# Optimization experiments

Measured on AMD Instinct MI355X. Metric: run time of the kernel, lower is better.

The kernel has to match this reference:

```python
import jax, jax.numpy as jnp
import numpy as np
from jax import lax


def _gru(x, h, Wih, Whh, bih, bhh):
    # PyTorch GRU cell: gates order (r, z, n)
    gi = x @ Wih.T + bih
    gh = h @ Whh.T + bhh
    ir, iz, inn = jnp.split(gi, 3, axis=-1)
    hr, hz, hn = jnp.split(gh, 3, axis=-1)
    r = jax.nn.sigmoid(ir + hr)
    z = jax.nn.sigmoid(iz + hz)
    n = jnp.tanh(inn + r * hn)
    return (1.0 - z) * n + z * h


def setup_inputs() -> dict:
    key = jax.random.key(0)
    ks = jax.random.split(key, 20)
    B, T, D, H, V, S = 128, 80, 4096, 1024, 6000, 10
    s = 0.02
    inp = {
        "data": jax.random.normal(ks[0], (B, T, D), dtype=jnp.float32),
        "mask": jnp.ones((B, S), dtype=jnp.float32),
        "target": jax.random.randint(ks[1], (B, S), 0, V),
        "sent_len": S,
        "enc_Wih": jax.random.normal(ks[2], (3 * H, D), dtype=jnp.float32) * s,
        "enc_Whh": jax.random.normal(ks[3], (3 * H, H), dtype=jnp.float32) * s,
        "enc_bih": jax.random.normal(ks[4], (3 * H,), dtype=jnp.float32) * s,
        "enc_bhh": jax.random.normal(ks[5], (3 * H,), dtype=jnp.float32) * s,
        "dec_Wih": jax.random.normal(ks[6], (3 * H, H), dtype=jnp.float32) * s,
        "dec_Whh": jax.random.normal(ks[7], (3 * H, H), dtype=jnp.float32) * s,
        "dec_bih": jax.random.normal(ks[8], (3 * H,), dtype=jnp.float32) * s,
        "dec_bhh": jax.random.normal(ks[9], (3 * H,), dtype=jnp.float32) * s,
        "lin1_W": jax.random.normal(ks[10], (H, 2 * H), dtype=jnp.float32) * s,
        "lin1_b": jnp.zeros((H,), dtype=jnp.float32),
        "lin2_W": jax.random.normal(ks[11], (V, H), dtype=jnp.float32) * s,
        "lin2_b": jnp.zeros((V,), dtype=jnp.float32),
        "embed": jax.random.normal(ks[12], (V, H), dtype=jnp.float32) * s,
    }
    return inp


def reference(data, mask, target, sent_len,
              enc_Wih, enc_Whh, enc_bih, enc_bhh,
              dec_Wih, dec_Whh, dec_bih, dec_bhh,
              lin1_W, lin1_b, lin2_W, lin2_b, embed):
    B = data.shape[0]
    H = lin1_b.shape[0]
    W1a = lin1_W[:, :H]   # acts on encoder hidden half
    W1b = lin1_W[:, H:]   # acts on embedded word half

    eh0 = jnp.zeros((B, H), dtype=data.dtype)
    dh0 = jnp.zeros((B, H), dtype=data.dtype)

    # ---- encode phase: feed video features; decoder sees [enc_hid, 0] ----
    def enc_step(carry, x_t):
        eh, dh = carry
        eh = _gru(x_t, eh, enc_Wih, enc_Whh, enc_bih, enc_bhh)
        u = jax.nn.relu(eh @ W1a.T + lin1_b)  # zeros half contributes nothing
        dh = _gru(u, dh, dec_Wih, dec_Whh, dec_bih, dec_bhh)
        return (eh, dh), None

    (eh, dh), _ = lax.scan(enc_step, (eh0, dh0), jnp.swapaxes(data, 0, 1))

    # ---- decode phase: encoder input is zeros; decoder sees [enc_hid, embed(word)] ----
    ir0, iz0, in0 = jnp.split(enc_bih, 3)  # zero-input encoder gates

    def dec_step(carry, tgt_t):
        eh, dh, word = carry
        gh = eh @ enc_Whh.T + enc_bhh
        hr, hz, hn = jnp.split(gh, 3, axis=-1)
        r = jax.nn.sigmoid(ir0 + hr)
        z = jax.nn.sigmoid(iz0 + hz)
        n = jnp.tanh(in0 + r * hn)
        eh = (1.0 - z) * n + z * eh

        emb = embed[word]  # [B, H]
        u = jax.nn.relu(eh @ W1a.T + emb @ W1b.T + lin1_b)
        dh = _gru(u, dh, dec_Wih, dec_Whh, dec_bih, dec_bhh)
        logp = jax.nn.log_softmax(dh @ lin2_W.T + lin2_b, axis=-1)  # [B, V]
        new_word = jnp.argmax(logp, axis=1).astype(jnp.int32)
        loss_t = -jnp.mean(logp[jnp.arange(B), tgt_t])  # NLLLoss (mask unused, as in source)
        return (eh, dh, new_word), (loss_t, new_word[0], new_word[1])

    word0 = jnp.ones((B,), dtype=jnp.int32)
    (_, _, _), (losses, sent, sent2) = lax.scan(dec_step, (eh, dh, word0), jnp.swapaxes(target, 0, 1))
    return jnp.sum(losses), sent, sent2
```

## Files before the change

kernel.cpp:

```cpp
#include <hip/hip_runtime.h>
#include <math.h>
#include <float.h>

#define B_ 128
#define T_ 80
#define D_ 4096
#define H_ 1024
#define V_ 6000
#define S_ 10
#define G3 (3*H_)
#define KSPLIT 4

typedef unsigned short ushort_t;
typedef __attribute__((ext_vector_type(8))) unsigned short u16x8;
typedef __attribute__((ext_vector_type(8))) short s16x8;
typedef __attribute__((ext_vector_type(4))) float fx4;

__device__ float    g_gi[(size_t)B_*T_*G3];
__device__ ushort_t g_Ah[(size_t)B_*T_*D_];
__device__ ushort_t g_Al[(size_t)B_*T_*D_];
__device__ ushort_t g_Bh[(size_t)G3*D_];
__device__ ushort_t g_Bl[(size_t)G3*D_];
__device__ float g_ghp [KSPLIT*B_*G3];
__device__ float g_gi2p[KSPLIT*B_*G3];
__device__ float g_gh2p[KSPLIT*B_*G3];
__device__ float g_up  [KSPLIT*B_*H_];
__device__ float g_eh[B_*H_];
__device__ float g_dh[B_*H_];
__device__ float g_u[B_*H_];
__device__ float g_cat[B_*2*H_];
__device__ float g_logits[B_*V_];
__device__ int   g_word[B_];

__device__ inline void split1(float x, ushort_t& hi, ushort_t& lo) {
    unsigned u = __float_as_uint(x);
    unsigned rh = u + 0x7FFF + ((u >> 16) & 1);
    hi = (ushort_t)(rh >> 16);
    float fhi = __uint_as_float((unsigned)hi << 16);
    float d = x - fhi;
    unsigned u2 = __float_as_uint(d);
    unsigned rl = u2 + 0x7FFF + ((u2 >> 16) & 1);
    lo = (ushort_t)(rl >> 16);
}

__global__ __launch_bounds__(256) void split_bf16(
    const float* __restrict__ x, ushort_t* __restrict__ hi,
    ushort_t* __restrict__ lo, int n4)
{
    int i = blockIdx.x * 256 + threadIdx.x;
    if (i >= n4) return;
    float4 v = ((const float4*)x)[i];
    ushort_t h0,h1,h2,h3,l0,l1,l2,l3;
    split1(v.x,h0,l0); split1(v.y,h1,l1); split1(v.z,h2,l2); split1(v.w,h3,l3);
    u16x8 dummy;
    ushort_t* hp = hi + (size_t)i*4;  hp[0]=h0; hp[1]=h1; hp[2]=h2; hp[3]=h3;
    ushort_t* lp = lo + (size_t)i*4;  lp[0]=l0; lp[1]=l1; lp[2]=l2; lp[3]=l3;
    (void)dummy;
}

__global__ __launch_bounds__(256) void gemm_mfma_x3(
    const ushort_t* __restrict__ Ahg, const ushort_t* __restrict__ Alg,
    const ushort_t* __restrict__ Bhg, const ushort_t* __restrict__ Blg,
    const float* __restrict__ bias, float* __restrict__ C, int N, int K)
{
    __shared__ ushort_t sAh[128*32], sAl[128*32], sBh[128*32], sBl[128*32];
    const int tid  = threadIdx.x;
    const int bm   = blockIdx.y * 128, bn = blockIdx.x * 128;
    const int wave = tid >> 6, lane = tid & 63;
    const int wr   = (wave >> 1) * 64, wc = (wave & 1) * 64;
    const int r    = lane & 15, g = lane >> 4;

    fx4 acc[4][4] = {};

    for (int k0 = 0; k0 < K; k0 += 32) {
        __syncthreads();
#pragma unroll
        for (int i = 0; i < 2; ++i) {
            const int o   = (tid + i*256) * 16;
            const int row = o >> 6;
            const int el  = (o & 63) >> 1;
            const size_t ga = (size_t)(bm + row) * K + k0 + el;
            const size_t gb = (size_t)(bn + row) * K + k0 + el;
            u16x8 vah = *(const u16x8*)(Ahg + ga);
            u16x8 val = *(const u16x8*)(Alg + ga);
            u16x8 vbh = *(const u16x8*)(Bhg + gb);
            u16x8 vbl = *(const u16x8*)(Blg + gb);
            const int lo2 = o >> 1;
            *(u16x8*)&sAh[lo2] = vah;
            *(u16x8*)&sAl[lo2] = val;
            *(u16x8*)&sBh[lo2] = vbh;
            *(u16x8*)&sBl[lo2] = vbl;
        }
        __syncthreads();

        s16x8 ah[4], al[4], bh[4], bl[4];
#pragma unroll
        for (int i = 0; i < 4; ++i) {
            const int ao = (wr + i*16 + r)*32 + g*8;
            const int bo = (wc + i*16 + r)*32 + g*8;
            ah[i] = *(const s16x8*)&sAh[ao];
            al[i] = *(const s16x8*)&sAl[ao];
            bh[i] = *(const s16x8*)&sBh[bo];
            bl[i] = *(const s16x8*)&sBl[bo];
        }
#pragma unroll
        for (int i = 0; i < 4; ++i)
#pragma unroll
            for (int j = 0; j < 4; ++j) {
                acc[i][j] = __builtin_amdgcn_mfma_f32_16x16x32_bf16(ah[i], bh[j], acc[i][j], 0, 0, 0);
                acc[i][j] = __builtin_amdgcn_mfma_f32_16x16x32_bf16(al[i], bh[j], acc[i][j], 0, 0, 0);
                acc[i][j] = __builtin_amdgcn_mfma_f32_16x16x32_bf16(ah[i], bl[j], acc[i][j], 0, 0, 0);
            }
    }

#pragma unroll
    for (int i = 0; i < 4; ++i)
#pragma unroll
        for (int j = 0; j < 4; ++j)
#pragma unroll
            for (int reg = 0; reg < 4; ++reg) {
                const int row = bm + wr + i*16 + g*4 + reg;
                const int col = bn + wc + j*16 + r;
                C[(size_t)row * N + col] = acc[i][j][reg] + bias[col];
            }
}

#define BM 64
#define BN 64
#define BK 16

__global__ __launch_bounds__(256) void gemm_wt(
    const float* __restrict__ A, int lda,
    const float* __restrict__ W, int ldw,
    const float* __restrict__ bias,
    float* __restrict__ C, int ldc,
    int M, int N, int K)
{
    __shared__ float As[BK][BM];
    __shared__ float Ws[BK][BN];
    const int tid = threadIdx.x;
    const int bm = blockIdx.y * BM;
    const int bn = blockIdx.x * BN;
    const int lr = tid >> 2;
    const int lc = (tid & 3) << 2;
    const int tr = (tid >> 4) << 2;
    const int tc = (tid & 15) << 2;

    float acc[4][4] = {};
    for (int k0 = 0; k0 < K; k0 += BK) {
        {
            const int gr = bm + lr;
            float4 av = *(const float4*)(A + (size_t)gr * lda + k0 + lc);
            As[lc+0][lr] = av.x; As[lc+1][lr] = av.y;
            As[lc+2][lr] = av.z; As[lc+3][lr] = av.w;
            const int wr2 = bn + lr;
            float4 wv = make_float4(0.f,0.f,0.f,0.f);
            if (wr2 < N) wv = *(const float4*)(W + (size_t)wr2 * ldw + k0 + lc);
            Ws[lc+0][lr] = wv.x; Ws[lc+1][lr] = wv.y;
            Ws[lc+2][lr] = wv.z; Ws[lc+3][lr] = wv.w;
        }
        __syncthreads();
#pragma unroll
        for (int k = 0; k < BK; ++k) {
            float4 a4 = *(const float4*)&As[k][tr];
            float4 b4 = *(const float4*)&Ws[k][tc];
            float ar[4] = {a4.x,a4.y,a4.z,a4.w};
            float br[4] = {b4.x,b4.y,b4.z,b4.w};
#pragma unroll
            for (int i = 0; i < 4; ++i)
#pragma unroll
                for (int j = 0; j < 4; ++j)
                    acc[i][j] = fmaf(ar[i], br[j], acc[i][j]);
        }
        __syncthreads();
    }
#pragma unroll
    for (int i = 0; i < 4; ++i) {
        const int m = bm + tr + i;
#pragma unroll
        for (int j = 0; j < 4; ++j) {
            const int n = bn + tc + j;
            if (n < N) C[(size_t)m * ldc + n] = acc[i][j] + bias[n];
        }
    }
}

__global__ __launch_bounds__(256) void gemm_wt_sk(
    const float* __restrict__ A, int lda,
    const float* __restrict__ W, int ldw,
    float* __restrict__ Cp,
    const float* __restrict__ A2,
    const float* __restrict__ W2,
    float* __restrict__ Cp2,
    int M, int N, int K)
{
    const int z = blockIdx.z;
    const int s = z & (KSPLIT - 1);
    if (z >= KSPLIT) { A = A2; W = W2; Cp = Cp2; }

    __shared__ float As[BK][BM];
    __shared__ float Ws[BK][BN];
    const int tid = threadIdx.x;
    const int bm = blockIdx.y * BM;
    const int bn = blockIdx.x * BN;
    const int lr = tid >> 2;
    const int lc = (tid & 3) << 2;
    const int tr = (tid >> 4) << 2;
    const int tc = (tid & 15) << 2;
    const int kc = K / KSPLIT;
    const int kbeg = s * kc;

    float acc[4][4] = {};
    for (int k0 = kbeg; k0 < kbeg + kc; k0 += BK) {
        {
            const int gr = bm + lr;
            float4 av = *(const float4*)(A + (size_t)gr * lda + k0 + lc);
            As[lc+0][lr] = av.x; As[lc+1][lr] = av.y;
            As[lc+2][lr] = av.z; As[lc+3][lr] = av.w;
            const int wr2 = bn + lr;
            float4 wv = *(const float4*)(W + (size_t)wr2 * ldw + k0 + lc);
            Ws[lc+0][lr] = wv.x; Ws[lc+1][lr] = wv.y;
            Ws[lc+2][lr] = wv.z; Ws[lc+3][lr] = wv.w;
        }
        __syncthreads();
#pragma unroll
        for (int k = 0; k < BK; ++k) {
            float4 a4 = *(const float4*)&As[k][tr];
            float4 b4 = *(const float4*)&Ws[k][tc];
            float ar[4] = {a4.x,a4.y,a4.z,a4.w};
            float br[4] = {b4.x,b4.y,b4.z,b4.w};
#pragma unroll
            for (int i = 0; i < 4; ++i)
#pragma unroll
                for (int j = 0; j < 4; ++j)
                    acc[i][j] = fmaf(ar[i], br[j], acc[i][j]);
        }
        __syncthreads();
    }
    float* Cs = Cp + (size_t)s * M * N;
#pragma unroll
    for (int i = 0; i < 4; ++i) {
        const int m = bm + tr + i;
#pragma unroll
        for (int j = 0; j < 4; ++j)
            Cs[(size_t)m * N + bn + tc + j] = acc[i][j];
    }
}

__global__ __launch_bounds__(256) void gru_update2(
    const float* __restrict__ GI, int gi_rstride, int gi_nsplit,
    const float* __restrict__ bih,
    const float* __restrict__ GHp, const float* __restrict__ bhh,
    float* __restrict__ h)
{
    const int idx = blockIdx.x * 256 + threadIdx.x;
    const int b = idx >> 10;
    const int j = idx & (H_ - 1);
    float ir, iz, inn;
    if (gi_nsplit == 0) {
        const float* gi = GI + (size_t)b * gi_rstride;
        ir = gi[j]; iz = gi[H_ + j]; inn = gi[2*H_ + j];
    } else {
        ir = bih[j]; iz = bih[H_ + j]; inn = bih[2*H_ + j];
        const float* p = GI + (size_t)b * G3;
#pragma unroll
        for (int s = 0; s < KSPLIT; ++s) {
            ir += p[j]; iz += p[H_ + j]; inn += p[2*H_ + j];
            p += (size_t)B_ * G3;
        }
    }
    float hr = bhh[j], hz = bhh[H_ + j], hn = bhh[2*H_ + j];
    const float* q = GHp + (size_t)b * G3;
#pragma unroll
    for (int s = 0; s < KSPLIT; ++s) {
        hr += q[j]; hz += q[H_ + j]; hn += q[2*H_ + j];
        q += (size_t)B_ * G3;
    }
    const float rg = 1.f / (1.f + expf(-(ir + hr)));
    const float zg = 1.f / (1.f + expf(-(iz + hz)));
    const float ng = tanhf(inn + rg * hn);
    h[idx] = (1.f - zg) * ng + zg * h[idx];
}

__global__ __launch_bounds__(256) void relu_combine(
    const float* __restrict__ Up, const float* __restrict__ bias,
    float* __restrict__ u)
{
    const int idx = blockIdx.x * 256 + threadIdx.x;
    const int j = idx & (H_ - 1);
    float v = bias[j];
#pragma unroll
    for (int s = 0; s < KSPLIT; ++s) v += Up[(size_t)s * B_ * H_ + idx];
    u[idx] = fmaxf(v, 0.f);
}

__global__ __launch_bounds__(256) void cat_eh_emb(
    const float* __restrict__ eh, const float* __restrict__ embed,
    const int* __restrict__ word, float* __restrict__ cat)
{
    const int idx = blockIdx.x * 256 + threadIdx.x;
    const int b = idx >> 11;
    const int j = idx & (2*H_ - 1);
    float v;
    if (j < H_) v = eh[b * H_ + j];
    else        v = embed[(size_t)word[b] * H_ + (j - H_)];
    cat[idx] = v;
}

__global__ __launch_bounds__(256) void init_state(
    float* __restrict__ eh, float* __restrict__ dh,
    int* __restrict__ word, float* __restrict__ out)
{
    const int idx = blockIdx.x * 256 + threadIdx.x;
    if (idx < B_*H_) { eh[idx] = 0.f; dh[idx] = 0.f; }
    if (idx < B_)    word[idx] = 1;
    if (idx < 21)    out[idx] = 0.f;
}

__global__ __launch_bounds__(256) void softmax_loss(
    const float* __restrict__ logits, const int* __restrict__ target,
    int s, int* __restrict__ word, float* __restrict__ out)
{
    const int b = blockIdx.x;
    const int t = threadIdx.x;
    const float* row = logits + (size_t)b * V_;
    __shared__ float sv[256];
    __shared__ int   si[256];
    __shared__ float ss[256];

    float best = -FLT_MAX; int bi = 0;
    for (int j = t; j < V_; j += 256) {
        float v = row[j];
        if (v > best) { best = v; bi = j; }
    }
    sv[t] = best; si[t] = bi;
    __syncthreads();
    for (int off = 128; off > 0; off >>= 1) {
        if (t < off) {
            float v2 = sv[t + off]; int i2 = si[t + off];
            if (v2 > sv[t] || (v2 == sv[t] && i2 < si[t])) { sv[t] = v2; si[t] = i2; }
        }
        __syncthreads();
    }
    const float m = sv[0];
    const int amax = si[0];

    float sum = 0.f;
    for (int j = t; j < V_; j += 256) sum += expf(row[j] - m);
    ss[t] = sum;
    __syncthreads();
    for (int off = 128; off > 0; off >>= 1) {
        if (t < off) ss[t] += ss[t + off];
        __syncthreads();
    }
    if (t == 0) {
        const float lse = m + logf(ss[0]);
        const int tgt = target[b * S_ + s];
        const float logp = row[tgt] - lse;
        atomicAdd(&out[0], -logp * (1.0f / (float)B_));
        word[b] = amax;
        if (b == 0) out[1 + s]  = (float)amax;
        if (b == 1) out[11 + s] = (float)amax;
    }
}

extern "C" void kernel_launch(void* const* d_in, const int* in_sizes, int n_in,
                              void* d_out, int out_size, void* d_ws, size_t ws_size,
                              hipStream_t stream)
{
    const float* data    = (const float*)d_in[0];
    const int*   target  = (const int*)  d_in[2];
    const float* enc_Wih = (const float*)d_in[4];
    const float* enc_Whh = (const float*)d_in[5];
    const float* enc_bih = (const float*)d_in[6];
    const float* enc_bhh = (const float*)d_in[7];
    const float* dec_Wih = (const float*)d_in[8];
    const float* dec_Whh = (const float*)d_in[9];
    const float* dec_bih = (const float*)d_in[10];
    const float* dec_bhh = (const float*)d_in[11];
    const float* lin1_W  = (const float*)d_in[12];
    const float* lin1_b  = (const float*)d_in[13];
    const float* lin2_W  = (const float*)d_in[14];
    const float* lin2_b  = (const float*)d_in[15];
    const float* embed   = (const float*)d_in[16];
    float* out = (float*)d_out;

    float *gi, *eh, *dh, *u, *cat, *logits, *ghp, *gi2p, *gh2p, *up;
    ushort_t *Ah, *Al, *Bh, *Bl; int* word;
    hipGetSymbolAddress((void**)&gi,     HIP_SYMBOL(g_gi));
    hipGetSymbolAddress((void**)&Ah,     HIP_SYMBOL(g_Ah));
    hipGetSymbolAddress((void**)&Al,     HIP_SYMBOL(g_Al));
    hipGetSymbolAddress((void**)&Bh,     HIP_SYMBOL(g_Bh));
    hipGetSymbolAddress((void**)&Bl,     HIP_SYMBOL(g_Bl));
    hipGetSymbolAddress((void**)&ghp,    HIP_SYMBOL(g_ghp));
    hipGetSymbolAddress((void**)&gi2p,   HIP_SYMBOL(g_gi2p));
    hipGetSymbolAddress((void**)&gh2p,   HIP_SYMBOL(g_gh2p));
    hipGetSymbolAddress((void**)&up,     HIP_SYMBOL(g_up));
    hipGetSymbolAddress((void**)&eh,     HIP_SYMBOL(g_eh));
    hipGetSymbolAddress((void**)&dh,     HIP_SYMBOL(g_dh));
    hipGetSymbolAddress((void**)&u,      HIP_SYMBOL(g_u));
    hipGetSymbolAddress((void**)&cat,    HIP_SYMBOL(g_cat));
    hipGetSymbolAddress((void**)&logits, HIP_SYMBOL(g_logits));
    hipGetSymbolAddress((void**)&word,   HIP_SYMBOL(g_word));

    init_state<<<512, 256, 0, stream>>>(eh, dh, word, out);

    split_bf16<<<(B_*T_*D_/4 + 255)/256, 256, 0, stream>>>(data,    Ah, Al, B_*T_*D_/4);
    split_bf16<<<(G3*D_/4   + 255)/256, 256, 0, stream>>>(enc_Wih, Bh, Bl, G3*D_/4);

    {
        dim3 grid(G3/128, (B_*T_)/128, 1);
        gemm_mfma_x3<<<grid, 256, 0, stream>>>(Ah, Al, Bh, Bl, enc_bih, gi, G3, D_);
    }

    for (int t = 0; t < T_; ++t) {
        { dim3 grid(G3/BN, B_/BM, KSPLIT);
          gemm_wt_sk<<<grid, 256, 0, stream>>>(eh, H_, enc_Whh, H_, ghp,
                                               nullptr, nullptr, nullptr, B_, G3, H_); }
        gru_update2<<<512, 256, 0, stream>>>(gi + (size_t)t * G3, T_ * G3, 0, nullptr,
                                             ghp, enc_bhh, eh);
        { dim3 grid(H_/BN, B_/BM, KSPLIT);
          gemm_wt_sk<<<grid, 256, 0, stream>>>(eh, H_, lin1_W, 2*H_, up,
                                               nullptr, nullptr, nullptr, B_, H_, H_); }
        relu_combine<<<512, 256, 0, stream>>>(up, lin1_b, u);
        { dim3 grid(G3/BN, B_/BM, 2*KSPLIT);
          gemm_wt_sk<<<grid, 256, 0, stream>>>(u, H_, dec_Wih, H_, gi2p,
                                               dh, dec_Whh, gh2p, B_, G3, H_); }
        gru_update2<<<512, 256, 0, stream>>>(gi2p, 0, KSPLIT, dec_bih,
                                             gh2p, dec_bhh, dh);
    }

    for (int s = 0; s < S_; ++s) {
        { dim3 grid(G3/BN, B_/BM, KSPLIT);
          gemm_wt_sk<<<grid, 256, 0, stream>>>(eh, H_, enc_Whh, H_, ghp,
                                               nullptr, nullptr, nullptr, B_, G3, H_); }
        gru_update2<<<512, 256, 0, stream>>>(enc_bih, 0, 0, nullptr,
                                             ghp, enc_bhh, eh);
        cat_eh_emb<<<1024, 256, 0, stream>>>(eh, embed, word, cat);
        { dim3 grid(H_/BN, B_/BM, KSPLIT);
          gemm_wt_sk<<<grid, 256, 0, stream>>>(cat, 2*H_, lin1_W, 2*H_, up,
                                               nullptr, nullptr, nullptr, B_, H_, 2*H_); }
        relu_combine<<<512, 256, 0, stream>>>(up, lin1_b, u);
        { dim3 grid(G3/BN, B_/BM, 2*KSPLIT);
          gemm_wt_sk<<<grid, 256, 0, stream>>>(u, H_, dec_Wih, H_, gi2p,
                                               dh, dec_Whh, gh2p, B_, G3, H_); }
        gru_update2<<<512, 256, 0, stream>>>(gi2p, 0, KSPLIT, dec_bih,
                                             gh2p, dec_bhh, dh);
        { dim3 grid((V_+BN-1)/BN, B_/BM, 1);
          gemm_wt<<<grid, 256, 0, stream>>>(dh, H_, lin2_W, H_, lin2_b, logits, V_, B_, V_, H_); }
        softmax_loss<<<B_, 256, 0, stream>>>(logits, target, s, word, out);
    }
}
```

Measured before the change: 8.728 ms.

## Move recurrent GEMMs to split-bf16 MFMA with double-buffered LDS loads

Replaces the fp32 FMA split-K GEMMs for the per-step recurrent matmuls with the 3-pass bf16 hi/lo MFMA kernel, generalized for split-K, leading dimensions and a dual-problem launch. Weights are pre-split once and hidden states are split inside the elementwise update kernels. The MFMA kernel now double-buffers shared memory using direct global-to-LDS loads, which should overlap loads with compute for the big input GEMM too. With M=128 the recurrent GEMMs launch few 128x128 tiles, so occupancy may be low, and the extra split work adds memory traffic.

```diff
diff --git a/kernel.cpp b/kernel.cpp
--- a/kernel.cpp
+++ b/kernel.cpp
@@ -12,7 +12,6 @@
 #define KSPLIT 4
 
 typedef unsigned short ushort_t;
-typedef __attribute__((ext_vector_type(8))) unsigned short u16x8;
 typedef __attribute__((ext_vector_type(8))) short s16x8;
 typedef __attribute__((ext_vector_type(4))) float fx4;
 
@@ -21,14 +20,20 @@
 __device__ ushort_t g_Al[(size_t)B_*T_*D_];
 __device__ ushort_t g_Bh[(size_t)G3*D_];
 __device__ ushort_t g_Bl[(size_t)G3*D_];
+__device__ ushort_t g_Whh_h[G3*H_],  g_Whh_l[G3*H_];
+__device__ ushort_t g_dWih_h[G3*H_], g_dWih_l[G3*H_];
+__device__ ushort_t g_dWhh_h[G3*H_], g_dWhh_l[G3*H_];
+__device__ ushort_t g_l1h[H_*2*H_],  g_l1l[H_*2*H_];
 __device__ float g_ghp [KSPLIT*B_*G3];
 __device__ float g_gi2p[KSPLIT*B_*G3];
 __device__ float g_gh2p[KSPLIT*B_*G3];
 __device__ float g_up  [KSPLIT*B_*H_];
 __device__ float g_eh[B_*H_];
 __device__ float g_dh[B_*H_];
-__device__ float g_u[B_*H_];
-__device__ float g_cat[B_*2*H_];
+__device__ ushort_t g_ehh[B_*H_], g_ehl[B_*H_];
+__device__ ushort_t g_dhh[B_*H_], g_dhl[B_*H_];
+__device__ ushort_t g_uh[B_*H_],  g_ul[B_*H_];
+__device__ ushort_t g_cath[B_*2*H_], g_catl[B_*2*H_];
 __device__ float g_logits[B_*V_];
 __device__ int   g_word[B_];
 
@@ -52,18 +57,33 @@
     float4 v = ((const float4*)x)[i];
     ushort_t h0,h1,h2,h3,l0,l1,l2,l3;
     split1(v.x,h0,l0); split1(v.y,h1,l1); split1(v.z,h2,l2); split1(v.w,h3,l3);
-    u16x8 dummy;
     ushort_t* hp = hi + (size_t)i*4;  hp[0]=h0; hp[1]=h1; hp[2]=h2; hp[3]=h3;
     ushort_t* lp = lo + (size_t)i*4;  lp[0]=l0; lp[1]=l1; lp[2]=l2; lp[3]=l3;
-    (void)dummy;
-}
-
-__global__ __launch_bounds__(256) void gemm_mfma_x3(
-    const ushort_t* __restrict__ Ahg, const ushort_t* __restrict__ Alg,
-    const ushort_t* __restrict__ Bhg, const ushort_t* __restrict__ Blg,
-    const float* __restrict__ bias, float* __restrict__ C, int N, int K)
-{
-    __shared__ ushort_t sAh[128*32], sAl[128*32], sBh[128*32], sBl[128*32];
+}
+
+__device__ inline void gld16(const ushort_t* g, void* l) {
+    __builtin_amdgcn_global_load_lds(
+        (const __attribute__((address_space(1))) void*)(const void*)g,
+        (__attribute__((address_space(3))) void*)l, 16, 0, 0);
+}
+
+__global__ __launch_bounds__(256) void gemm_x3(
+    const ushort_t* __restrict__ Ah, const ushort_t* __restrict__ Al, int lda,
+    const ushort_t* __restrict__ Bh, const ushort_t* __restrict__ Bl, int ldw,
+    const float* __restrict__ bias,
+    float* __restrict__ C,
+    int M, int N, int K, int kchunks,
+    const ushort_t* __restrict__ A2h, const ushort_t* __restrict__ A2l,
+    const ushort_t* __restrict__ B2h, const ushort_t* __restrict__ B2l,
+    float* __restrict__ C2)
+{
+    int z = blockIdx.z;
+    int kc = z;
+    if (z >= kchunks) { kc = z - kchunks; Ah=A2h; Al=A2l; Bh=B2h; Bl=B2l; C=C2; }
+
+    __shared__ ushort_t sAh[2][128*32], sAl[2][128*32];
+    __shared__ ushort_t sBh[2][128*32], sBl[2][128*32];
+
     const int tid  = threadIdx.x;
     const int bm   = blockIdx.y * 128, bn = blockIdx.x * 128;
     const int wave = tid >> 6, lane = tid & 63;
@@ -72,47 +92,58 @@
 
     fx4 acc[4][4] = {};
 
-    for (int k0 = 0; k0 < K; k0 += 32) {
-        __syncthreads();
-#pragma unroll
-        for (int i = 0; i < 2; ++i) {
-            const int o   = (tid + i*256) * 16;
-            const int row = o >> 6;
-            const int el  = (o & 63) >> 1;
-            const size_t ga = (size_t)(bm + row) * K + k0 + el;
-            const size_t gb = (size_t)(bn + row) * K + k0 + el;
-            u16x8 vah = *(const u16x8*)(Ahg + ga);
-            u16x8 val = *(const u16x8*)(Alg + ga);
-            u16x8 vbh = *(const u16x8*)(Bhg + gb);
-            u16x8 vbl = *(const u16x8*)(Blg + gb);
-            const int lo2 = o >> 1;
-            *(u16x8*)&sAh[lo2] = vah;
-            *(u16x8*)&sAl[lo2] = val;
-            *(u16x8*)&sBh[lo2] = vbh;
-            *(u16x8*)&sBl[lo2] = vbl;
-        }
-        __syncthreads();
-
-        s16x8 ah[4], al[4], bh[4], bl[4];
+    const int kper = K / kchunks;
+    const int kbeg = kc * kper;
+    const int nt   = kper / 32;
+
+#define STAGE(buf, k0)                                                        \
+    {                                                                         \
+      _Pragma("unroll")                                                       \
+      for (int i_ = 0; i_ < 2; ++i_) {                                        \
+        const int o_   = (tid + i_*256) * 16;    \
+        const int row_ = o_ >> 6;                                             \
+        const int el_  = (o_ & 63) >> 1;                                      \
+        const size_t ga_ = (size_t)(bm + row_) * lda + (k0) + el_;            \
+        const size_t gb_ = (size_t)(bn + row_) * ldw + (k0) + el_;            \
+        const int lb_ = (wave*64 + i_*256) * 16;   \
+        gld16(Ah + ga_, (char*)&sAh[buf][0] + lb_);                           \
+        gld16(Al + ga_, (char*)&sAl[buf][0] + lb_);                           \
+        gld16(Bh + gb_, (char*)&sBh[buf][0] + lb_);                           \
+        gld16(Bl + gb_, (char*)&sBl[buf][0] + lb_);                           \
+      }                                                                       \
+    }
+
+    int cur = 0;
+    STAGE(0, kbeg)
+    __syncthreads();
+
+    for (int t = 0; t < nt; ++t) {
+        if (t + 1 < nt) STAGE(cur ^ 1, kbeg + (t+1)*32)
+
+        s16x8 a_h[4], a_l[4], b_h[4], b_l[4];
 #pragma unroll
         for (int i = 0; i < 4; ++i) {
             const int ao = (wr + i*16 + r)*32 + g*8;
             const int bo = (wc + i*16 + r)*32 + g*8;
-            ah[i] = *(const s16x8*)&sAh[ao];
-            al[i] = *(const s16x8*)&sAl[ao];
-            bh[i] = *(const s16x8*)&sBh[bo];
-            bl[i] = *(const s16x8*)&sBl[bo];
+            a_h[i] = *(const s16x8*)&sAh[cur][ao];
+            a_l[i] = *(const s16x8*)&sAl[cur][ao];
+            b_h[i] = *(const s16x8*)&sBh[cur][bo];
+            b_l[i] = *(const s16x8*)&sBl[cur][bo];
         }
 #pragma unroll
         for (int i = 0; i < 4; ++i)
 #pragma unroll
             for (int j = 0; j < 4; ++j) {
-                acc[i][j] = __builtin_amdgcn_mfma_f32_16x16x32_bf16(ah[i], bh[j], acc[i][j], 0, 0, 0);
-                acc[i][j] = __builtin_amdgcn_mfma_f32_16x16x32_bf16(al[i], bh[j], acc[i][j], 0, 0, 0);
-                acc[i][j] = __builtin_amdgcn_mfma_f32_16x16x32_bf16(ah[i], bl[j], acc[i][j], 0, 0, 0);
+                acc[i][j] = __builtin_amdgcn_mfma_f32_16x16x32_bf16(a_h[i], b_h[j], acc[i][j], 0, 0, 0);
+                acc[i][j] = __builtin_amdgcn_mfma_f32_16x16x32_bf16(a_l[i], b_h[j], acc[i][j], 0, 0, 0);
+                acc[i][j] = __builtin_amdgcn_mfma_f32_16x16x32_bf16(a_h[i], b_l[j], acc[i][j], 0, 0, 0);
             }
-    }
-
+        __syncthreads();
+        cur ^= 1;
+    }
+#undef STAGE
+
+    float* Cw = C + (size_t)kc * M * N;
 #pragma unroll
     for (int i = 0; i < 4; ++i)
 #pragma unroll
@@ -121,7 +152,9 @@
             for (int reg = 0; reg < 4; ++reg) {
                 const int row = bm + wr + i*16 + g*4 + reg;
                 const int col = bn + wc + j*16 + r;
-                C[(size_t)row * N + col] = acc[i][j][reg] + bias[col];
+                float v = acc[i][j][reg];
+                if (kchunks == 1 && bias) v += bias[col];
+                Cw[(size_t)row * N + col] = v;
             }
 }
 
@@ -185,73 +218,11 @@
     }
 }
 
-__global__ __launch_bounds__(256) void gemm_wt_sk(
-    const float* __restrict__ A, int lda,
-    const float* __restrict__ W, int ldw,
-    float* __restrict__ Cp,
-    const float* __restrict__ A2,
-    const float* __restrict__ W2,
-    float* __restrict__ Cp2,
-    int M, int N, int K)
-{
-    const int z = blockIdx.z;
-    const int s = z & (KSPLIT - 1);
-    if (z >= KSPLIT) { A = A2; W = W2; Cp = Cp2; }
-
-    __shared__ float As[BK][BM];
-    __shared__ float Ws[BK][BN];
-    const int tid = threadIdx.x;
-    const int bm = blockIdx.y * BM;
-    const int bn = blockIdx.x * BN;
-    const int lr = tid >> 2;
-    const int lc = (tid & 3) << 2;
-    const int tr = (tid >> 4) << 2;
-    const int tc = (tid & 15) << 2;
-    const int kc = K / KSPLIT;
-    const int kbeg = s * kc;
-
-    float acc[4][4] = {};
-    for (int k0 = kbeg; k0 < kbeg + kc; k0 += BK) {
-        {
-            const int gr = bm + lr;
-            float4 av = *(const float4*)(A + (size_t)gr * lda + k0 + lc);
-            As[lc+0][lr] = av.x; As[lc+1][lr] = av.y;
-            As[lc+2][lr] = av.z; As[lc+3][lr] = av.w;
-            const int wr2 = bn + lr;
-            float4 wv = *(const float4*)(W + (size_t)wr2 * ldw + k0 + lc);
-            Ws[lc+0][lr] = wv.x; Ws[lc+1][lr] = wv.y;
-            Ws[lc+2][lr] = wv.z; Ws[lc+3][lr] = wv.w;
-        }
-        __syncthreads();
-#pragma unroll
-        for (int k = 0; k < BK; ++k) {
-            float4 a4 = *(const float4*)&As[k][tr];
-            float4 b4 = *(const float4*)&Ws[k][tc];
-            float ar[4] = {a4.x,a4.y,a4.z,a4.w};
-            float br[4] = {b4.x,b4.y,b4.z,b4.w};
-#pragma unroll
-            for (int i = 0; i < 4; ++i)
-#pragma unroll
-                for (int j = 0; j < 4; ++j)
-                    acc[i][j] = fmaf(ar[i], br[j], acc[i][j]);
-        }
-        __syncthreads();
-    }
-    float* Cs = Cp + (size_t)s * M * N;
-#pragma unroll
-    for (int i = 0; i < 4; ++i) {
-        const int m = bm + tr + i;
-#pragma unroll
-        for (int j = 0; j < 4; ++j)
-            Cs[(size_t)m * N + bn + tc + j] = acc[i][j];
-    }
-}
-
 __global__ __launch_bounds__(256) void gru_update2(
     const float* __restrict__ GI, int gi_rstride, int gi_nsplit,
     const float* __restrict__ bih,
     const float* __restrict__ GHp, const float* __restrict__ bhh,
-    float* __restrict__ h)
+    float* __restrict__ h, ushort_t* __restrict__ hh, ushort_t* __restrict__ hl)
 {
     const int idx = blockIdx.x * 256 + threadIdx.x;
     const int b = idx >> 10;
@@ -279,40 +250,52 @@
     const float rg = 1.f / (1.f + expf(-(ir + hr)));
     const float zg = 1.f / (1.f + expf(-(iz + hz)));
     const float ng = tanhf(inn + rg * hn);
-    h[idx] = (1.f - zg) * ng + zg * h[idx];
+    const float v = (1.f - zg) * ng + zg * h[idx];
+    h[idx] = v;
+    split1(v, hh[idx], hl[idx]);
 }
 
 __global__ __launch_bounds__(256) void relu_combine(
     const float* __restrict__ Up, const float* __restrict__ bias,
-    float* __restrict__ u)
+    ushort_t* __restrict__ uh, ushort_t* __restrict__ ul)
 {
     const int idx = blockIdx.x * 256 + threadIdx.x;
     const int j = idx & (H_ - 1);
     float v = bias[j];
 #pragma unroll
     for (int s = 0; s < KSPLIT; ++s) v += Up[(size_t)s * B_ * H_ + idx];
-    u[idx] = fmaxf(v, 0.f);
+    v = fmaxf(v, 0.f);
+    split1(v, uh[idx], ul[idx]);
 }
 
 __global__ __launch_bounds__(256) void cat_eh_emb(
-    const float* __restrict__ eh, const float* __restrict__ embed,
-    const int* __restrict__ word, float* __restrict__ cat)
+    const ushort_t* __restrict__ ehh, const ushort_t* __restrict__ ehl,
+    const float* __restrict__ embed, const int* __restrict__ word,
+    ushort_t* __restrict__ cath, ushort_t* __restrict__ catl)
 {
     const int idx = blockIdx.x * 256 + threadIdx.x;
     const int b = idx >> 11;
     const int j = idx & (2*H_ - 1);
-    float v;
-    if (j < H_) v = eh[b * H_ + j];
-    else        v = embed[(size_t)word[b] * H_ + (j - H_)];
-    cat[idx] = v;
+    if (j < H_) {
+        cath[idx] = ehh[b * H_ + j];
+        catl[idx] = ehl[b * H_ + j];
+    } else {
+        float v = embed[(size_t)word[b] * H_ + (j - H_)];
+        split1(v, cath[idx], catl[idx]);
+    }
 }
 
 __global__ __launch_bounds__(256) void init_state(
     float* __restrict__ eh, float* __restrict__ dh,
+    ushort_t* __restrict__ ehh, ushort_t* __restrict__ ehl,
+    ushort_t* __restrict__ dhh, ushort_t* __restrict__ dhl,
     int* __restrict__ word, float* __restrict__ out)
 {
     const int idx = blockIdx.x * 256 + threadIdx.x;
-    if (idx < B_*H_) { eh[idx] = 0.f; dh[idx] = 0.f; }
+    if (idx < B_*H_) {
+        eh[idx] = 0.f; dh[idx] = 0.f;
+        ehh[idx] = 0; ehl[idx] = 0; dhh[idx] = 0; dhl[idx] = 0;
+    }
     if (idx < B_)    word[idx] = 1;
     if (idx < 21)    out[idx] = 0.f;
 }
@@ -362,6 +345,28 @@
         if (b == 0) out[1 + s]  = (float)amax;
         if (b == 1) out[11 + s] = (float)amax;
     }
+}
+
+static inline void launch_x3(hipStream_t st,
+    const ushort_t* Ah, const ushort_t* Al, int lda,
+    const ushort_t* Bh, const ushort_t* Bl, int ldw,
+    const float* bias, float* C, int M, int N, int K, int kchunks)
+{
+    dim3 grid(N/128, M/128, kchunks);
+    gemm_x3<<<grid, 256, 0, st>>>(Ah, Al, lda, Bh, Bl, ldw, bias, C, M, N, K, kchunks,
+                                  nullptr, nullptr, nullptr, nullptr, nullptr);
+}
+
+static inline void launch_x3_dual(hipStream_t st,
+    const ushort_t* Ah, const ushort_t* Al,
+    const ushort_t* Bh, const ushort_t* Bl, float* C,
+    const ushort_t* A2h, const ushort_t* A2l,
+    const ushort_t* B2h, const ushort_t* B2l, float* C2,
+    int M, int N, int K, int kchunks)
+{
+    dim3 grid(N/128, M/128, 2*kchunks);
+    gemm_x3<<<grid, 256, 0, st>>>(Ah, Al, H_, Bh, Bl, H_, nullptr, C, M, N, K, kchunks,
+                                  A2h, A2l, B2h, B2l, C2);
 }
 
 extern "C" void kernel_launch(void* const* d_in, const int* in_sizes, int n_in,
@@ -385,67 +390,74 @@
     const float* embed   = (const float*)d_in[16];
     float* out = (float*)d_out;
 
-    float *gi, *eh, *dh, *u, *cat, *logits, *ghp, *gi2p, *gh2p, *up;
-    ushort_t *Ah, *Al, *Bh, *Bl; int* word;
+    float *gi, *eh, *dh, *logits, *ghp, *gi2p, *gh2p, *up;
+    ushort_t *Ah, *Al, *Bh, *Bl, *Whh_h, *Whh_l, *dWih_h, *dWih_l, *dWhh_h, *dWhh_l;
+    ushort_t *l1h, *l1l, *ehh, *ehl, *dhh, *dhl, *uh, *ul, *cath, *catl;
+    int* word;
     hipGetSymbolAddress((void**)&gi,     HIP_SYMBOL(g_gi));
     hipGetSymbolAddress((void**)&Ah,     HIP_SYMBOL(g_Ah));
     hipGetSymbolAddress((void**)&Al,     HIP_SYMBOL(g_Al));
     hipGetSymbolAddress((void**)&Bh,     HIP_SYMBOL(g_Bh));
     hipGetSymbolAddress((void**)&Bl,     HIP_SYMBOL(g_Bl));
+    hipGetSymbolAddress((void**)&Whh_h,  HIP_SYMBOL(g_Whh_h));
+    hipGetSymbolAddress((void**)&Whh_l,  HIP_SYMBOL(g_Whh_l));
+    hipGetSymbolAddress((void**)&dWih_h, HIP_SYMBOL(g_dWih_h));
+    hipGetSymbolAddress((void**)&dWih_l, HIP_SYMBOL(g_dWih_l));
+    hipGetSymbolAddress((void**)&dWhh_h, HIP_SYMBOL(g_dWhh_h));
+    hipGetSymbolAddress((void**)&dWhh_l, HIP_SYMBOL(g_dWhh_l));
+    hipGetSymbolAddress((void**)&l1h,    HIP_SYMBOL(g_l1h));
+    hipGetSymbolAddress((void**)&l1l,    HIP_SYMBOL(g_l1l));
     hipGetSymbolAddress((void**)&ghp,    HIP_SYMBOL(g_ghp));
     hipGetSymbolAddress((void**)&gi2p,   HIP_SYMBOL(g_gi2p));
     hipGetSymbolAddress((void**)&gh2p,   HIP_SYMBOL(g_gh2p));
     hipGetSymbolAddress((void**)&up,     HIP_SYMBOL(g_up));
     hipGetSymbolAddress((void**)&eh,     HIP_SYMBOL(g_eh));
     hipGetSymbolAddress((void**)&dh,     HIP_SYMBOL(g_dh));
-    hipGetSymbolAddress((void**)&u,      HIP_SYMBOL(g_u));
-    hipGetSymbolAddress((void**)&cat,    HIP_SYMBOL(g_cat));
+    hipGetSymbolAddress((void**)&ehh,    HIP_SYMBOL(g_ehh));
+    hipGetSymbolAddress((void**)&ehl,    HIP_SYMBOL(g_ehl));
+    hipGetSymbolAddress((void**)&dhh,    HIP_SYMBOL(g_dhh));
+    hipGetSymbolAddress((void**)&dhl,    HIP_SYMBOL(g_dhl));
+    hipGetSymbolAddress((void**)&uh,     HIP_SYMBOL(g_uh));
+    hipGetSymbolAddress((void**)&ul,     HIP_SYMBOL(g_ul));
+    hipGetSymbolAddress((void**)&cath,   HIP_SYMBOL(g_cath));
+    hipGetSymbolAddress((void**)&catl,   HIP_SYMBOL(g_catl));
     hipGetSymbolAddress((void**)&logits, HIP_SYMBOL(g_logits));
     hipGetSymbolAddress((void**)&word,   HIP_SYMBOL(g_word));
 
-    init_state<<<512, 256, 0, stream>>>(eh, dh, word, out);
+    init_state<<<512, 256, 0, stream>>>(eh, dh, ehh, ehl, dhh, dhl, word, out);
 
     split_bf16<<<(B_*T_*D_/4 + 255)/256, 256, 0, stream>>>(data,    Ah, Al, B_*T_*D_/4);
     split_bf16<<<(G3*D_/4   + 255)/256, 256, 0, stream>>>(enc_Wih, Bh, Bl, G3*D_/4);
-
-    {
-        dim3 grid(G3/128, (B_*T_)/128, 1);
-        gemm_mfma_x3<<<grid, 256, 0, stream>>>(Ah, Al, Bh, Bl, enc_bih, gi, G3, D_);
-    }
+    split_bf16<<<(G3*H_/4   + 255)/256, 256, 0, stream>>>(enc_Whh, Whh_h, Whh_l, G3*H_/4);
+    split_bf16<<<(G3*H_/4   + 255)/256, 256, 0, stream>>>(dec_Wih, dWih_h, dWih_l, G3*H_/4);
+    split_bf16<<<(G3*H_/4   + 255)/256, 256, 0, stream>>>(dec_Whh, dWhh_h, dWhh_l, G3*H_/4);
+    split_bf16<<<(H_*2*H_/4 + 255)/256, 256, 0, stream>>>(lin1_W,  l1h, l1l, H_*2*H_/4);
+
+    launch_x3(stream, Ah, Al, D_, Bh, Bl, D_, enc_bih, gi, B_*T_, G3, D_, 1);
 
     for (int t = 0; t < T_; ++t) {
-        { dim3 grid(G3/BN, B_/BM, KSPLIT);
-          gemm_wt_sk<<<grid, 256, 0, stream>>>(eh, H_, enc_Whh, H_, ghp,
-                                               nullptr, nullptr, nullptr, B_, G3, H_); }
+        launch_x3(stream, ehh, ehl, H_, Whh_h, Whh_l, H_, nullptr, ghp, B_, G3, H_, KSPLIT);
         gru_update2<<<512, 256, 0, stream>>>(gi + (size_t)t * G3, T_ * G3, 0, nullptr,
-                                             ghp, enc_bhh, eh);
-        { dim3 grid(H_/BN, B_/BM, KSPLIT);
-          gemm_wt_sk<<<grid, 256, 0, stream>>>(eh, H_, lin1_W, 2*H_, up,
-                                               nullptr, nullptr, nullptr, B_, H_, H_); }
-        relu_combine<<<512, 256, 0, stream>>>(up, lin1_b, u);
-        { dim3 grid(G3/BN, B_/BM, 2*KSPLIT);
-          gemm_wt_sk<<<grid, 256, 0, stream>>>(u, H_, dec_Wih, H_, gi2p,
-                                               dh, dec_Whh, gh2p, B_, G3, H_); }
+                                             ghp, enc_bhh, eh, ehh, ehl);
+        launch_x3(stream, ehh, ehl, H_, l1h, l1l, 2*H_, nullptr, up, B_, H_, H_, KSPLIT);
+        relu_combine<<<512, 256, 0, stream>>>(up, lin1_b, uh, ul);
+        launch_x3_dual(stream, uh, ul, dWih_h, dWih_l, gi2p,
+                               dhh, dhl, dWhh_h, dWhh_l, gh2p, B_, G3, H_, KSPLIT);
         gru_update2<<<512, 256, 0, stream>>>(gi2p, 0, KSPLIT, dec_bih,
-                                             gh2p, dec_bhh, dh);
+                                             gh2p, dec_bhh, dh, dhh, dhl);
     }
 
     for (int s = 0; s < S_; ++s) {
-        { dim3 grid(G3/BN, B_/BM, KSPLIT);
-          gemm_wt_sk<<<grid, 256, 0, stream>>>(eh, H_, enc_Whh, H_, ghp,
-                                               nullptr, nullptr, nullptr, B_, G3, H_); }
+        launch_x3(stream, ehh, ehl, H_, Whh_h, Whh_l, H_, nullptr, ghp, B_, G3, H_, KSPLIT);
         gru_update2<<<512, 256, 0, stream>>>(enc_bih, 0, 0, nullptr,
-                                             ghp, enc_bhh, eh);
-        cat_eh_emb<<<1024, 256, 0, stream>>>(eh, embed, word, cat);
-        { dim3 grid(H_/BN, B_/BM, KSPLIT);
-          gemm_wt_sk<<<grid, 256, 0, stream>>>(cat, 2*H_, lin1_W, 2*H_, up,
-                                               nullptr, nullptr, nullptr, B_, H_, 2*H_); }
-        relu_combine<<<512, 256, 0, stream>>>(up, lin1_b, u);
-        { dim3 grid(G3/BN, B_/BM, 2*KSPLIT);
-          gemm_wt_sk<<<grid, 256, 0, stream>>>(u, H_, dec_Wih, H_, gi2p,
-                                               dh, dec_Whh, gh2p, B_, G3, H_); }
+                                             ghp, enc_bhh, eh, ehh, ehl);
+        cat_eh_emb<<<1024, 256, 0, stream>>>(ehh, ehl, embed, word, cath, catl);
+        launch_x3(stream, cath, catl, 2*H_, l1h, l1l, 2*H_, nullptr, up, B_, H_, 2*H_, KSPLIT);
+        relu_combine<<<512, 256, 0, stream>>>(up, lin1_b, uh, ul);
+        launch_x3_dual(stream, uh, ul, dWih_h, dWih_l, gi2p,
+                               dhh, dhl, dWhh_h, dWhh_l, gh2p, B_, G3, H_, KSPLIT);
         gru_update2<<<512, 256, 0, stream>>>(gi2p, 0, KSPLIT, dec_bih,
-                                             gh2p, dec_bhh, dh);
+                                             gh2p, dec_bhh, dh, dhh, dhl);
         { dim3 grid((V_+BN-1)/BN, B_/BM, 1);
           gemm_wt<<<grid, 256, 0, stream>>>(dh, H_, lin2_W, H_, lin2_b, logits, V_, B_, V_, H_); }
         softmax_loss<<<B_, 256, 0, stream>>>(logits, target, s, word, out);
```

Measured after the change: 7.508 ms. 1.16x faster.
